# Kernel optimization log

Measured on AMD Instinct MI355X. Metric: run time of the kernel, lower is better.

Reference implementation:

```python
import jax, jax.numpy as jnp
import numpy as np

B, T, E, H, D = 2, 1024, 2048, 16, 64
DEPTH = 12
LAMBDA_INIT = 0.8 - 0.6 * float(np.exp(-0.3 * DEPTH))
EPS = 1e-5


def _rope_interleaved(x):
    # x: (b, t, heads, d), rotate interleaved even/odd pairs
    d = x.shape[-1]
    inv_freq = 1.0 / (10000.0 ** (jnp.arange(0, d, 2, dtype=jnp.float32) / d))  # (d/2,)
    ang = jnp.arange(x.shape[1], dtype=jnp.float32)[:, None] * inv_freq[None, :]  # (t, d/2)
    cos = jnp.cos(ang)[None, :, None, :].astype(x.dtype)
    sin = jnp.sin(ang)[None, :, None, :].astype(x.dtype)
    x1, x2 = x[..., 0::2], x[..., 1::2]
    r1 = x1 * cos - x2 * sin
    r2 = x1 * sin + x2 * cos
    return jnp.stack([r1, r2], axis=-1).reshape(x.shape)


def setup_inputs() -> dict:
    key = jax.random.key(0)
    ks = jax.random.split(key, 11)
    w_scale = 0.02
    return {
        "x": jax.random.normal(ks[0], (B, T, E), jnp.float32),
        "rel_pos": jax.random.uniform(ks[1], (T, D), jnp.float32),
        "wq": jax.random.normal(ks[2], (E, E), jnp.float32) * w_scale,
        "wk": jax.random.normal(ks[3], (E, E), jnp.float32) * w_scale,
        "wv": jax.random.normal(ks[4], (E, E), jnp.float32) * w_scale,
        "lambda_q1": jax.random.normal(ks[5], (D,), jnp.float32) * 0.1,
        "lambda_q2": jax.random.normal(ks[6], (D,), jnp.float32) * 0.1,
        "lambda_k1": jax.random.normal(ks[7], (D,), jnp.float32) * 0.1,
        "lambda_k2": jax.random.normal(ks[8], (D,), jnp.float32) * 0.1,
        "subln_w": jnp.ones((2 * D,), jnp.float32),
        "wo": jax.random.normal(ks[9], (E, E), jnp.float32) * w_scale,
    }


def reference(x, rel_pos, wq, wk, wv, lambda_q1, lambda_q2, lambda_k1, lambda_k2, subln_w, wo):
    b, t, e = x.shape
    scaling = D ** 0.5
    # projections; q,k have 2*H heads of dim D, v has H heads of dim 2*D
    q = (x @ wq.T).reshape(b, t, 2 * H, D)
    k = (x @ wk.T).reshape(b, t, 2 * H, D)
    v = (x @ wv.T).reshape(b, t, H, 2 * D)
    k = k * rel_pos[None, :, None, :]
    q = _rope_interleaved(q)
    k = _rope_interleaved(k)
    q = q.transpose(0, 2, 1, 3)  # (b, 2H, t, D)
    k = k.transpose(0, 2, 1, 3)
    v = v.transpose(0, 2, 1, 3)  # (b, H, t, 2D)
    scores = jnp.einsum("bhqd,bhkd->bhqk", q, k) / scaling
    causal = jnp.tril(jnp.ones((t, t), bool))
    scores = jnp.where(causal[None, None], scores, jnp.float32(-1e9))
    p = jax.nn.softmax(scores.astype(jnp.float32), axis=-1).astype(x.dtype)
    lam1 = jnp.exp(jnp.sum(lambda_q1 * lambda_k1))
    lam2 = jnp.exp(jnp.sum(lambda_q2 * lambda_k2))
    lam_full = lam1 - lam2 + LAMBDA_INIT
    p = p.reshape(b, H, 2, t, t)
    pw = p[:, :, 0] - lam_full * p[:, :, 1]  # (b, H, t, t)
    attn = jnp.einsum("bhqk,bhkd->bhqd", pw, v)  # (b, H, t, 2D)
    # RMSNorm over last dim (2D)
    ms = jnp.mean(attn.astype(jnp.float32) ** 2, axis=-1, keepdims=True)
    attn = (attn * jax.lax.rsqrt(ms + EPS)).astype(x.dtype) * subln_w
    out = attn.transpose(0, 2, 1, 3).reshape(b, t, H * 2 * D) @ wo.T
    return out
```

## Files before the change

kernel.cpp:

```cpp
#include <hip/hip_runtime.h>

typedef __bf16 bf16x8 __attribute__((ext_vector_type(8)));
typedef float f32x4 __attribute__((ext_vector_type(4)));

__device__ __forceinline__ float bf2f(unsigned short u) {
  return __uint_as_float(((unsigned)u) << 16);
}
__device__ __forceinline__ unsigned short f2bf(float f) {
  unsigned u = __float_as_uint(f);
  return (unsigned short)((u + 0x7fffu + ((u >> 16) & 1u)) >> 16);
}
__device__ __forceinline__ unsigned pack2(float a, float b) {
  return (unsigned)f2bf(a) | ((unsigned)f2bf(b) << 16);
}

#define SWZB(row, byte) ((byte) ^ (((row) & 7) << 4))

#define AS_GLOBAL(p) ((const __attribute__((address_space(1))) void*)(p))
#define AS_LDS(p) ((__attribute__((address_space(3))) void*)(p))

__global__ void lambda_kernel(const float* __restrict__ lq1, const float* __restrict__ lq2,
                              const float* __restrict__ lk1, const float* __restrict__ lk2,
                              float* __restrict__ out, float lam_init) {
  int l = threadIdx.x;
  float p1 = lq1[l] * lk1[l];
  float p2 = lq2[l] * lk2[l];
  #pragma unroll
  for (int off = 32; off; off >>= 1) {
    p1 += __shfl_xor(p1, off);
    p2 += __shfl_xor(p2, off);
  }
  if (l == 0) out[0] = expf(p1) - expf(p2) + lam_init;
}

__global__ __launch_bounds__(256) void cvt_f32_bf16(const float* __restrict__ in,
                                                    unsigned short* __restrict__ out, int n4) {
  int idx = blockIdx.x * 256 + threadIdx.x;
  if (idx >= n4) return;
  float4 v = reinterpret_cast<const float4*>(in)[idx];
  uint2 pk;
  pk.x = pack2(v.x, v.y);
  pk.y = pack2(v.z, v.w);
  reinterpret_cast<uint2*>(out)[idx] = pk;
}

template <typename OT>
__global__ __launch_bounds__(256)
void gemm_lds(const unsigned short* __restrict__ A, const unsigned short* __restrict__ Bw,
              OT* __restrict__ C, int M, int K, int ldc) {
  __shared__ __align__(16) unsigned short As[128 * 32];
  __shared__ __align__(16) unsigned short Bs[128 * 32];
  const int tid = threadIdx.x;
  const int bm = blockIdx.x * 128, bn = blockIdx.y * 128;
  const int lane = tid & 63, wave = tid >> 6;
  const int wm = (wave >> 1) * 64, wn = (wave & 1) * 64;
  const int kf = (lane >> 4) * 8, rr = lane & 15;
  const int ldrow = lane >> 2, ldk = (lane & 3) * 8;
  OT* Cb = C + (size_t)(bn / ldc) * ((size_t)M * ldc) + (bn % ldc);
  f32x4 acc[4][4] = {};
  for (int kt = 0; kt < K; kt += 32) {
    __syncthreads();
    #pragma unroll
    for (int i = 0; i < 2; ++i) {
      int row = (i * 4 + wave) * 16 + ldrow;
      __builtin_amdgcn_global_load_lds(AS_GLOBAL(&A[(long)(bm + row) * K + kt + ldk]),
                                       AS_LDS(&As[(i * 4 + wave) * 512]), 16, 0, 0);
      __builtin_amdgcn_global_load_lds(AS_GLOBAL(&Bw[(long)(bn + row) * K + kt + ldk]),
                                       AS_LDS(&Bs[(i * 4 + wave) * 512]), 16, 0, 0);
    }
    __syncthreads();
    bf16x8 af[4], bq[4];
    #pragma unroll
    for (int i = 0; i < 4; ++i)
      af[i] = *reinterpret_cast<const bf16x8*>(&As[(wm + i * 16 + rr) * 32 + kf]);
    #pragma unroll
    for (int j = 0; j < 4; ++j)
      bq[j] = *reinterpret_cast<const bf16x8*>(&Bs[(wn + j * 16 + rr) * 32 + kf]);
    #pragma unroll
    for (int i = 0; i < 4; ++i)
      #pragma unroll
      for (int j = 0; j < 4; ++j)
        acc[i][j] = __builtin_amdgcn_mfma_f32_16x16x32_bf16(af[i], bq[j], acc[i][j], 0, 0, 0);
  }
  const int r0 = (lane >> 4) * 4, c0 = lane & 15;
  #pragma unroll
  for (int i = 0; i < 4; ++i)
    #pragma unroll
    for (int j = 0; j < 4; ++j) {
      #pragma unroll
      for (int r = 0; r < 4; ++r) {
        long row = bm + wm + i * 16 + r0 + r;
        long col = wn + j * 16 + c0;
        float v = acc[i][j][r];
        if constexpr (sizeof(OT) == 2) Cb[row * ldc + col] = f2bf(v);
        else                           Cb[row * ldc + col] = v;
      }
    }
}

__global__ __launch_bounds__(256) void rope_kernel(const unsigned short* __restrict__ raw,
                                                   const float* __restrict__ rel,
                                                   unsigned short* __restrict__ out,
                                                   int use_rel) {
  int idx = blockIdx.x * 256 + threadIdx.x;
  int i = idx & 31;
  int t = (idx >> 5) & 1023;
  int hp = (idx >> 15) & 31;
  int b = idx >> 20;
  int src = (b * 1024 + t) * 2048 + hp * 64 + 2 * i;
  unsigned pair = *reinterpret_cast<const unsigned*>(&raw[src]);
  float x1 = __uint_as_float(pair << 16);
  float x2 = __uint_as_float(pair & 0xffff0000u);
  if (use_rel) {
    x1 *= rel[t * 64 + 2 * i];
    x2 *= rel[t * 64 + 2 * i + 1];
  }
  float inv = expf(-0.28782313662425574f * (float)i);
  float ang = (float)t * inv;
  float s, c;
  sincosf(ang, &s, &c);
  float r1 = x1 * c - x2 * s;
  float r2 = x1 * s + x2 * c;
  int dst = ((b * 32 + hp) * 1024 + t) * 64 + 2 * i;
  *reinterpret_cast<unsigned*>(&out[dst]) = pack2(r1, r2);
}

__global__ __launch_bounds__(256) void transpose_v(const unsigned short* __restrict__ in,
                                                   unsigned short* __restrict__ out) {
  __shared__ unsigned short ls[64][68];
  const int t0 = blockIdx.x * 64, n0 = blockIdx.y * 64, b = blockIdx.z;
  const int tid = threadIdx.x;
  #pragma unroll
  for (int p = 0; p < 4; ++p) {
    int idx = p * 256 + tid;
    int tl = idx >> 4, nq = (idx & 15) * 4;
    *reinterpret_cast<uint2*>(&ls[tl][nq]) = *reinterpret_cast<const uint2*>(
        &in[((long)(b * 1024 + t0 + tl)) * 2048 + n0 + nq]);
  }
  __syncthreads();
  #pragma unroll
  for (int p = 0; p < 4; ++p) {
    int idx = p * 256 + tid;
    int nl = idx >> 4, tq = (idx & 15) * 4;
    unsigned short a0 = ls[tq + 0][nl], a1 = ls[tq + 1][nl];
    unsigned short a2 = ls[tq + 2][nl], a3 = ls[tq + 3][nl];
    uint2 o;
    o.x = (unsigned)a0 | ((unsigned)a1 << 16);
    o.y = (unsigned)a2 | ((unsigned)a3 << 16);
    *reinterpret_cast<uint2*>(&out[((long)(b * 2048 + n0 + nl)) * 1024 + t0 + tq]) = o;
  }
}

__global__ __launch_bounds__(256) void attn_mfma(
    const unsigned short* __restrict__ Qa,
    const unsigned short* __restrict__ Ka,
    const unsigned short* __restrict__ Vt,
    const float* __restrict__ lam_p,
    const float* __restrict__ subln,
    unsigned short* __restrict__ O) {
  const int n = blockIdx.x;
  const int c = n & 7, m = n >> 3;
  const int g = c * 4 + (m >> 4);
  const int bx = m & 15;
  const int h = g & 15, b = g >> 4;

  const int tid = threadIdx.x;
  const int lane = tid & 63, w = tid >> 6;
  const int lg = lane >> 4, cc = lane & 15;
  const int hh = w >> 1, qoff = (w & 1) * 16;

  __shared__ __align__(16) unsigned short KsBuf[2][2 * 64 * 64];
  __shared__ __align__(16) unsigned short VsBuf[2][128 * 64];
  __shared__ __align__(16) unsigned short PbBuf[4 * 16 * 64];

  const float lam = lam_p[0];
  char* ksb0 = reinterpret_cast<char*>(&KsBuf[0][0]);
  char* vsb0 = reinterpret_cast<char*>(&VsBuf[0][0]);
  char* pbb = reinterpret_cast<char*>(PbBuf) + w * 2048;
  float* cb = reinterpret_cast<float*>(&KsBuf[0][0]);

  const int srow = lane >> 3;
  const int sblk = (lane & 7) ^ srow;
  auto STAGE = [&](char* kd, char* vd, int k0) {
    #pragma unroll
    for (int j = 0; j < 4; ++j) {
      int s = w * 4 + j;
      int sh = s >> 3, rg = s & 7;
      const unsigned short* ksrc =
          &Ka[(((long)(b * 32 + 2 * h + sh)) * 1024 + k0 + rg * 8 + srow) * 64 + sblk * 8];
      __builtin_amdgcn_global_load_lds(AS_GLOBAL(ksrc), AS_LDS(kd + sh * 8192 + rg * 1024),
                                       16, 0, 0);
      const unsigned short* vsrc =
          &Vt[((long)(b * 2048 + h * 128 + s * 8 + srow)) * 1024 + k0 + sblk * 8];
      __builtin_amdgcn_global_load_lds(AS_GLOBAL(vsrc), AS_LDS(vd + s * 1024), 16, 0, 0);
    }
  };

  float sl[8];
  #pragma unroll
  for (int jc = 0; jc < 8; ++jc) sl[jc] = subln[jc * 16 + cc];

  const long kbase = (long)((b * 32 + 2 * h + hh) * 1024);

  for (int pass = 0; pass < 2; ++pass) {
    const int q0 = (pass ? (31 - bx) : bx) * 32;
    const int nt = ((q0 + 31) >> 6) + 1;

    __syncthreads();
    STAGE(ksb0, vsb0, 0);

    bf16x8 qf[2];
    {
      const long qrow = q0 + qoff + cc;
      #pragma unroll
      for (int c2 = 0; c2 < 2; ++c2)
        qf[c2] = *reinterpret_cast<const bf16x8*>(&Qa[(kbase + qrow) * 64 + c2 * 32 + lg * 8]);
    }
    f32x4 acc_o[8];
    float mS[4], lS[4];
    #pragma unroll
    for (int jc = 0; jc < 8; ++jc) acc_o[jc] = (f32x4){0.f, 0.f, 0.f, 0.f};
    #pragma unroll
    for (int r = 0; r < 4; ++r) { mS[r] = -1e30f; lS[r] = 0.f; }

    __syncthreads();

    int cur = 0;
    for (int tile = 0; tile < nt; ++tile) {
      if (tile + 1 < nt)
        STAGE(ksb0 + (cur ^ 1) * 16384, vsb0 + (cur ^ 1) * 16384, (tile + 1) * 64);
      char* kb = ksb0 + cur * 16384;
      char* vb = vsb0 + cur * 16384;

      const int k0 = tile * 64;
      f32x4 s4[4];
      #pragma unroll
      for (int j = 0; j < 4; ++j) s4[j] = (f32x4){0.f, 0.f, 0.f, 0.f};
      #pragma unroll
      for (int j = 0; j < 4; ++j) {
        int row = j * 16 + cc;
        const char* base = kb + hh * 8192 + row * 128;
        bf16x8 kb0 = *reinterpret_cast<const bf16x8*>(base + SWZB(row, lg * 16));
        bf16x8 kb1 = *reinterpret_cast<const bf16x8*>(base + SWZB(row, lg * 16 + 64));
        s4[j] = __builtin_amdgcn_mfma_f32_16x16x32_bf16(qf[0], kb0, s4[j], 0, 0, 0);
        s4[j] = __builtin_amdgcn_mfma_f32_16x16x32_bf16(qf[1], kb1, s4[j], 0, 0, 0);
      }
      #pragma unroll
      for (int j = 0; j < 4; ++j) {
        int kcol = k0 + j * 16 + cc;
        #pragma unroll
        for (int r = 0; r < 4; ++r) {
          int qrow = q0 + qoff + lg * 4 + r;
          float s = s4[j][r] * 0.125f;
          s4[j][r] = (kcol > qrow) ? -1e30f : s;
        }
      }
      float rescv[4];
      #pragma unroll
      for (int r = 0; r < 4; ++r) {
        float mx = fmaxf(fmaxf(s4[0][r], s4[1][r]), fmaxf(s4[2][r], s4[3][r]));
        mx = fmaxf(mx, __shfl_xor(mx, 1));
        mx = fmaxf(mx, __shfl_xor(mx, 2));
        mx = fmaxf(mx, __shfl_xor(mx, 4));
        mx = fmaxf(mx, __shfl_xor(mx, 8));
        float mold = mS[r];
        float mnew = fmaxf(mold, mx);
        mS[r] = mnew;
        float rsc = __expf(mold - mnew);
        rescv[r] = rsc;
        float ls = 0.f;
        #pragma unroll
        for (int j = 0; j < 4; ++j) {
          float p = __expf(s4[j][r] - mnew);
          s4[j][r] = p;
          ls += p;
        }
        ls += __shfl_xor(ls, 1);
        ls += __shfl_xor(ls, 2);
        ls += __shfl_xor(ls, 4);
        ls += __shfl_xor(ls, 8);
        lS[r] = lS[r] * rsc + ls;
      }
      #pragma unroll
      for (int j = 0; j < 4; ++j)
        #pragma unroll
        for (int r = 0; r < 4; ++r) {
          int rowl = lg * 4 + r;
          *reinterpret_cast<unsigned short*>(
              pbb + rowl * 128 + SWZB(rowl, (j * 16 + cc) * 2)) = f2bf(s4[j][r]);
        }

      bf16x8 pa[2];
      #pragma unroll
      for (int c2 = 0; c2 < 2; ++c2)
        pa[c2] = *reinterpret_cast<const bf16x8*>(pbb + cc * 128 + SWZB(cc, lg * 16 + c2 * 64));
      #pragma unroll
      for (int jc = 0; jc < 8; ++jc)
        #pragma unroll
        for (int r = 0; r < 4; ++r)
          acc_o[jc][r] *= rescv[r];
      #pragma unroll
      for (int jc = 0; jc < 8; ++jc) {
        int row = jc * 16 + cc;
        const char* base = vb + row * 128;
        bf16x8 vf0 = *reinterpret_cast<const bf16x8*>(base + SWZB(row, lg * 16));
        bf16x8 vf1 = *reinterpret_cast<const bf16x8*>(base + SWZB(row, lg * 16 + 64));
        acc_o[jc] = __builtin_amdgcn_mfma_f32_16x16x32_bf16(pa[0], vf0, acc_o[jc], 0, 0, 0);
        acc_o[jc] = __builtin_amdgcn_mfma_f32_16x16x32_bf16(pa[1], vf1, acc_o[jc], 0, 0, 0);
      }

      __syncthreads();
      cur ^= 1;
    }

    if (hh == 1) {
      #pragma unroll
      for (int r = 0; r < 4; ++r) {
        float inv2 = lam / lS[r];
        int row = qoff + lg * 4 + r;
        #pragma unroll
        for (int jc = 0; jc < 8; ++jc)
          cb[row * 128 + ((jc ^ (row & 7)) * 16 + cc)] = acc_o[jc][r] * inv2;
      }
    }
    __syncthreads();
    if (hh == 0) {
      float sc[4];
      #pragma unroll
      for (int r = 0; r < 4; ++r) {
        float inv1 = 1.f / lS[r];
        int row = qoff + lg * 4 + r;
        float ss = 0.f;
        #pragma unroll
        for (int jc = 0; jc < 8; ++jc) {
          float at = acc_o[jc][r] * inv1 - cb[row * 128 + ((jc ^ (row & 7)) * 16 + cc)];
          acc_o[jc][r] = at;
          ss += at * at;
        }
        ss += __shfl_xor(ss, 1);
        ss += __shfl_xor(ss, 2);
        ss += __shfl_xor(ss, 4);
        ss += __shfl_xor(ss, 8);
        sc[r] = rsqrtf(ss * (1.f / 128.f) + 1e-5f);
      }
      #pragma unroll
      for (int r = 0; r < 4; ++r) {
        long qrow = q0 + qoff + lg * 4 + r;
        #pragma unroll
        for (int jc = 0; jc < 8; ++jc) {
          O[(long)(b * 1024 + qrow) * 2048 + h * 128 + jc * 16 + cc] =
              f2bf(acc_o[jc][r] * sc[r] * sl[jc]);
        }
      }
    }
  }
}

extern "C" void kernel_launch(void* const* d_in, const int* in_sizes, int n_in,
                              void* d_out, int out_size, void* d_ws, size_t ws_size,
                              hipStream_t stream) {
  (void)in_sizes; (void)n_in; (void)out_size; (void)ws_size;
  const float* x    = (const float*)d_in[0];
  const float* rel  = (const float*)d_in[1];
  const float* wq   = (const float*)d_in[2];
  const float* wk   = (const float*)d_in[3];
  const float* wv   = (const float*)d_in[4];
  const float* lq1  = (const float*)d_in[5];
  const float* lq2  = (const float*)d_in[6];
  const float* lk1  = (const float*)d_in[7];
  const float* lk2  = (const float*)d_in[8];
  const float* subw = (const float*)d_in[9];
  const float* wo   = (const float*)d_in[10];
  float* out = (float*)d_out;

  char* ws = (char*)d_ws;
  const size_t SZ = (size_t)2048 * 2048 * 2;
  unsigned short* qraw  = (unsigned short*)(ws);
  unsigned short* kraw  = (unsigned short*)(ws + SZ);
  unsigned short* vraw  = (unsigned short*)(ws + 2 * SZ);
  unsigned short* xbf   = (unsigned short*)(ws + 3 * SZ);
  unsigned short* wqkvb = (unsigned short*)(ws + 4 * SZ);
  unsigned short* qatt  = (unsigned short*)(ws + 4 * SZ);
  unsigned short* katt  = (unsigned short*)(ws + 5 * SZ);
  unsigned short* wob   = (unsigned short*)(ws + 6 * SZ);
  float* lamb           = (float*)(ws + 7 * SZ);
  unsigned short* vtb  = kraw;
  unsigned short* aout = qraw;

  lambda_kernel<<<1, 64, 0, stream>>>(lq1, lq2, lk1, lk2, lamb, 0.7836057665316245f);

  const int N4 = 2048 * 2048 / 4;
  cvt_f32_bf16<<<N4 / 256, 256, 0, stream>>>(x, xbf, N4);
  cvt_f32_bf16<<<N4 / 256, 256, 0, stream>>>(wq, wqkvb, N4);
  cvt_f32_bf16<<<N4 / 256, 256, 0, stream>>>(wk, wqkvb + (size_t)2048 * 2048, N4);
  cvt_f32_bf16<<<N4 / 256, 256, 0, stream>>>(wv, wqkvb + (size_t)2 * 2048 * 2048, N4);

  gemm_lds<unsigned short><<<dim3(16, 48), 256, 0, stream>>>(xbf, wqkvb, qraw, 2048, 2048, 2048);

  rope_kernel<<<8192, 256, 0, stream>>>(qraw, rel, qatt, 0);
  rope_kernel<<<8192, 256, 0, stream>>>(kraw, rel, katt, 1);
  cvt_f32_bf16<<<N4 / 256, 256, 0, stream>>>(wo, wob, N4);

  transpose_v<<<dim3(16, 32, 2), 256, 0, stream>>>(vraw, vtb);

  attn_mfma<<<dim3(512), 256, 0, stream>>>(qatt, katt, vtb, lamb, subw, aout);

  gemm_lds<float><<<dim3(16, 16), 256, 0, stream>>>(aout, wob, out, 2048, 2048, 2048);
}
```

Before: 216.8 us.

## Fuse RoPE into QKV GEMM epilogue, widen K tile to 64, batch conversions

The QKV projection GEMM now applies rel_pos scaling and interleaved RoPE in its epilogue, pairing neighbouring columns with a lane shuffle and writing head-major Q/K directly. This removes the two separate rope passes and the bf16 round trip of raw Q/K. The GEMM K-tile grows from 32 to 64 and uses an XOR-swizzled LDS layout to avoid bank conflicts. The four f32->bf16 conversions are merged into one launch, and the workspace layout is reshuffled to fit. The cost is sincosf and expf evaluated per accumulator element in the epilogue, plus more LDS per block.

```diff
diff --git a/kernel.cpp b/kernel.cpp
--- a/kernel.cpp
+++ b/kernel.cpp
@@ -44,85 +44,124 @@
   reinterpret_cast<uint2*>(out)[idx] = pk;
 }
 
-template <typename OT>
+__global__ __launch_bounds__(256) void cvt4_f32_bf16(
+    const float* __restrict__ s0, const float* __restrict__ s1,
+    const float* __restrict__ s2, const float* __restrict__ s3,
+    unsigned short* __restrict__ d0, unsigned short* __restrict__ d1,
+    unsigned short* __restrict__ d2, unsigned short* __restrict__ d3, int n4) {
+  int idx = blockIdx.x * 256 + threadIdx.x;
+  if (idx >= n4) return;
+  const float* s;
+  unsigned short* d;
+  switch (blockIdx.y) {
+    case 0: s = s0; d = d0; break;
+    case 1: s = s1; d = d1; break;
+    case 2: s = s2; d = d2; break;
+    default: s = s3; d = d3; break;
+  }
+  float4 v = reinterpret_cast<const float4*>(s)[idx];
+  uint2 pk;
+  pk.x = pack2(v.x, v.y);
+  pk.y = pack2(v.z, v.w);
+  reinterpret_cast<uint2*>(d)[idx] = pk;
+}
+
+template <int EPI>
 __global__ __launch_bounds__(256)
-void gemm_lds(const unsigned short* __restrict__ A, const unsigned short* __restrict__ Bw,
-              OT* __restrict__ C, int M, int K, int ldc) {
-  __shared__ __align__(16) unsigned short As[128 * 32];
-  __shared__ __align__(16) unsigned short Bs[128 * 32];
+void gemm_bk64(const unsigned short* __restrict__ A, const unsigned short* __restrict__ Bw,
+               float* __restrict__ C, unsigned short* __restrict__ Qd,
+               unsigned short* __restrict__ Kd, unsigned short* __restrict__ Vd,
+               const float* __restrict__ rel, int M, int K, int ldc) {
+  __shared__ __align__(16) unsigned short As[128 * 64];
+  __shared__ __align__(16) unsigned short Bs[128 * 64];
   const int tid = threadIdx.x;
   const int bm = blockIdx.x * 128, bn = blockIdx.y * 128;
   const int lane = tid & 63, wave = tid >> 6;
   const int wm = (wave >> 1) * 64, wn = (wave & 1) * 64;
-  const int kf = (lane >> 4) * 8, rr = lane & 15;
-  const int ldrow = lane >> 2, ldk = (lane & 3) * 8;
-  OT* Cb = C + (size_t)(bn / ldc) * ((size_t)M * ldc) + (bn % ldc);
+  const int rr = lane & 15, lg = lane >> 4;
+  const int srow = lane >> 3;
+  const int sblk = (lane & 7) ^ srow;
+  const char* ab = reinterpret_cast<const char*>(As);
+  const char* bb = reinterpret_cast<const char*>(Bs);
   f32x4 acc[4][4] = {};
-  for (int kt = 0; kt < K; kt += 32) {
+  for (int kt = 0; kt < K; kt += 64) {
     __syncthreads();
     #pragma unroll
-    for (int i = 0; i < 2; ++i) {
-      int row = (i * 4 + wave) * 16 + ldrow;
-      __builtin_amdgcn_global_load_lds(AS_GLOBAL(&A[(long)(bm + row) * K + kt + ldk]),
-                                       AS_LDS(&As[(i * 4 + wave) * 512]), 16, 0, 0);
-      __builtin_amdgcn_global_load_lds(AS_GLOBAL(&Bw[(long)(bn + row) * K + kt + ldk]),
-                                       AS_LDS(&Bs[(i * 4 + wave) * 512]), 16, 0, 0);
+    for (int j = 0; j < 4; ++j) {
+      int s = wave + j * 4;
+      const unsigned short* asrc = &A[(long)(bm + s * 8 + srow) * K + kt + sblk * 8];
+      __builtin_amdgcn_global_load_lds(AS_GLOBAL(asrc), AS_LDS(&As[s * 512]), 16, 0, 0);
+      const unsigned short* bsrc = &Bw[(long)(bn + s * 8 + srow) * K + kt + sblk * 8];
+      __builtin_amdgcn_global_load_lds(AS_GLOBAL(bsrc), AS_LDS(&Bs[s * 512]), 16, 0, 0);
     }
     __syncthreads();
-    bf16x8 af[4], bq[4];
+    bf16x8 af[4][2], bq[4][2];
+    #pragma unroll
+    for (int i = 0; i < 4; ++i) {
+      int row = wm + i * 16 + rr;
+      af[i][0] = *reinterpret_cast<const bf16x8*>(ab + row * 128 + SWZB(row, lg * 16));
+      af[i][1] = *reinterpret_cast<const bf16x8*>(ab + row * 128 + SWZB(row, 64 + lg * 16));
+    }
+    #pragma unroll
+    for (int j = 0; j < 4; ++j) {
+      int row = wn + j * 16 + rr;
+      bq[j][0] = *reinterpret_cast<const bf16x8*>(bb + row * 128 + SWZB(row, lg * 16));
+      bq[j][1] = *reinterpret_cast<const bf16x8*>(bb + row * 128 + SWZB(row, 64 + lg * 16));
+    }
     #pragma unroll
     for (int i = 0; i < 4; ++i)
-      af[i] = *reinterpret_cast<const bf16x8*>(&As[(wm + i * 16 + rr) * 32 + kf]);
-    #pragma unroll
-    for (int j = 0; j < 4; ++j)
-      bq[j] = *reinterpret_cast<const bf16x8*>(&Bs[(wn + j * 16 + rr) * 32 + kf]);
+      #pragma unroll
+      for (int j = 0; j < 4; ++j) {
+        acc[i][j] = __builtin_amdgcn_mfma_f32_16x16x32_bf16(af[i][0], bq[j][0], acc[i][j], 0, 0, 0);
+        acc[i][j] = __builtin_amdgcn_mfma_f32_16x16x32_bf16(af[i][1], bq[j][1], acc[i][j], 0, 0, 0);
+      }
+  }
+  const int cc = lane & 15;
+  if constexpr (EPI == 0) {
     #pragma unroll
     for (int i = 0; i < 4; ++i)
       #pragma unroll
       for (int j = 0; j < 4; ++j)
-        acc[i][j] = __builtin_amdgcn_mfma_f32_16x16x32_bf16(af[i], bq[j], acc[i][j], 0, 0, 0);
-  }
-  const int r0 = (lane >> 4) * 4, c0 = lane & 15;
-  #pragma unroll
-  for (int i = 0; i < 4; ++i)
-    #pragma unroll
-    for (int j = 0; j < 4; ++j) {
-      #pragma unroll
-      for (int r = 0; r < 4; ++r) {
-        long row = bm + wm + i * 16 + r0 + r;
-        long col = wn + j * 16 + c0;
-        float v = acc[i][j][r];
-        if constexpr (sizeof(OT) == 2) Cb[row * ldc + col] = f2bf(v);
-        else                           Cb[row * ldc + col] = v;
-      }
-    }
-}
-
-__global__ __launch_bounds__(256) void rope_kernel(const unsigned short* __restrict__ raw,
-                                                   const float* __restrict__ rel,
-                                                   unsigned short* __restrict__ out,
-                                                   int use_rel) {
-  int idx = blockIdx.x * 256 + threadIdx.x;
-  int i = idx & 31;
-  int t = (idx >> 5) & 1023;
-  int hp = (idx >> 15) & 31;
-  int b = idx >> 20;
-  int src = (b * 1024 + t) * 2048 + hp * 64 + 2 * i;
-  unsigned pair = *reinterpret_cast<const unsigned*>(&raw[src]);
-  float x1 = __uint_as_float(pair << 16);
-  float x2 = __uint_as_float(pair & 0xffff0000u);
-  if (use_rel) {
-    x1 *= rel[t * 64 + 2 * i];
-    x2 *= rel[t * 64 + 2 * i + 1];
-  }
-  float inv = expf(-0.28782313662425574f * (float)i);
-  float ang = (float)t * inv;
-  float s, c;
-  sincosf(ang, &s, &c);
-  float r1 = x1 * c - x2 * s;
-  float r2 = x1 * s + x2 * c;
-  int dst = ((b * 32 + hp) * 1024 + t) * 64 + 2 * i;
-  *reinterpret_cast<unsigned*>(&out[dst]) = pack2(r1, r2);
+        #pragma unroll
+        for (int r = 0; r < 4; ++r)
+          C[(long)(bm + wm + i * 16 + lg * 4 + r) * ldc + bn + wn + j * 16 + cc] = acc[i][j][r];
+  } else {
+    const int proj = bn >> 11;
+    const int nbase = bn & 2047;
+    if (proj == 2) {
+      #pragma unroll
+      for (int i = 0; i < 4; ++i)
+        #pragma unroll
+        for (int j = 0; j < 4; ++j)
+          #pragma unroll
+          for (int r = 0; r < 4; ++r)
+            Vd[(long)(bm + wm + i * 16 + lg * 4 + r) * 2048 + nbase + wn + j * 16 + cc] =
+                f2bf(acc[i][j][r]);
+    } else {
+      unsigned short* D = (proj == 0) ? Qd : Kd;
+      #pragma unroll
+      for (int j = 0; j < 4; ++j) {
+        int n = nbase + wn + j * 16 + cc;
+        int hp = n >> 6, dd = n & 63;
+        float invf = expf(-0.28782313662425574f * (float)(dd >> 1));
+        #pragma unroll
+        for (int i = 0; i < 4; ++i) {
+          #pragma unroll
+          for (int r = 0; r < 4; ++r) {
+            int m = bm + wm + i * 16 + lg * 4 + r;
+            int t = m & 1023, bb2 = m >> 10;
+            float val = acc[i][j][r];
+            if (proj == 1) val *= rel[t * 64 + dd];
+            float p = __shfl_xor(val, 1);
+            float s, cth;
+            sincosf((float)t * invf, &s, &cth);
+            float ro = (cc & 1) ? fmaf(p, s, val * cth) : fmaf(val, cth, -p * s);
+            D[((long)(bb2 * 32 + hp) * 1024 + t) * 64 + dd] = f2bf(ro);
+          }
+        }
+      }
+    }
+  }
 }
 
 __global__ __launch_bounds__(256) void transpose_v(const unsigned short* __restrict__ in,
@@ -375,35 +414,32 @@
 
   char* ws = (char*)d_ws;
   const size_t SZ = (size_t)2048 * 2048 * 2;
-  unsigned short* qraw  = (unsigned short*)(ws);
-  unsigned short* kraw  = (unsigned short*)(ws + SZ);
-  unsigned short* vraw  = (unsigned short*)(ws + 2 * SZ);
+  unsigned short* wqkvb = (unsigned short*)(ws);
+  unsigned short* vtb   = (unsigned short*)(ws);
+  unsigned short* aout  = (unsigned short*)(ws + SZ);
+  unsigned short* wob   = (unsigned short*)(ws + 2 * SZ);
   unsigned short* xbf   = (unsigned short*)(ws + 3 * SZ);
-  unsigned short* wqkvb = (unsigned short*)(ws + 4 * SZ);
   unsigned short* qatt  = (unsigned short*)(ws + 4 * SZ);
   unsigned short* katt  = (unsigned short*)(ws + 5 * SZ);
-  unsigned short* wob   = (unsigned short*)(ws + 6 * SZ);
+  unsigned short* vraw  = (unsigned short*)(ws + 6 * SZ);
   float* lamb           = (float*)(ws + 7 * SZ);
-  unsigned short* vtb  = kraw;
-  unsigned short* aout = qraw;
 
   lambda_kernel<<<1, 64, 0, stream>>>(lq1, lq2, lk1, lk2, lamb, 0.7836057665316245f);
 
   const int N4 = 2048 * 2048 / 4;
-  cvt_f32_bf16<<<N4 / 256, 256, 0, stream>>>(x, xbf, N4);
-  cvt_f32_bf16<<<N4 / 256, 256, 0, stream>>>(wq, wqkvb, N4);
-  cvt_f32_bf16<<<N4 / 256, 256, 0, stream>>>(wk, wqkvb + (size_t)2048 * 2048, N4);
-  cvt_f32_bf16<<<N4 / 256, 256, 0, stream>>>(wv, wqkvb + (size_t)2 * 2048 * 2048, N4);
-
-  gemm_lds<unsigned short><<<dim3(16, 48), 256, 0, stream>>>(xbf, wqkvb, qraw, 2048, 2048, 2048);
-
-  rope_kernel<<<8192, 256, 0, stream>>>(qraw, rel, qatt, 0);
-  rope_kernel<<<8192, 256, 0, stream>>>(kraw, rel, katt, 1);
+  cvt4_f32_bf16<<<dim3(N4 / 256, 4), 256, 0, stream>>>(
+      x, wq, wk, wv, xbf, wqkvb, wqkvb + (size_t)2048 * 2048,
+      wqkvb + (size_t)2 * 2048 * 2048, N4);
+
+  gemm_bk64<1><<<dim3(16, 48), 256, 0, stream>>>(xbf, wqkvb, nullptr, qatt, katt, vraw,
+                                                 rel, 2048, 2048, 0);
+
   cvt_f32_bf16<<<N4 / 256, 256, 0, stream>>>(wo, wob, N4);
 
   transpose_v<<<dim3(16, 32, 2), 256, 0, stream>>>(vraw, vtb);
 
   attn_mfma<<<dim3(512), 256, 0, stream>>>(qatt, katt, vtb, lamb, subw, aout);
 
-  gemm_lds<float><<<dim3(16, 16), 256, 0, stream>>>(aout, wob, out, 2048, 2048, 2048);
-}
+  gemm_bk64<0><<<dim3(16, 16), 256, 0, stream>>>(aout, wob, out, nullptr, nullptr, nullptr,
+                                                 nullptr, 2048, 2048, 2048);
+}
```

After: 547.0 us. +152.3%, slower.
